# Performance work log

Hardware: AMD Instinct MI355X
Metric: run time of the kernel (lower is better)

Reference implementation:

```python
import jax, jax.numpy as jnp
import numpy as np

B, C, H, W = 8, 384, 32, 32
HEADS, DIM_HEAD = 6, 64
INNER = HEADS * DIM_HEAD  # 384


def setup_inputs() -> dict:
    key = jax.random.key(0)
    ks = jax.random.split(key, 6)
    s = 0.02
    return {
        "query": jax.random.normal(ks[0], (B, C, H, W), jnp.float32),
        "context": jax.random.normal(ks[1], (B, C, H, W), jnp.float32),
        "Wq": jax.random.normal(ks[2], (INNER, C), jnp.float32) * s,
        "Wk": jax.random.normal(ks[3], (INNER, C), jnp.float32) * s,
        "Wv": jax.random.normal(ks[4], (INNER, C), jnp.float32) * s,
        "Wo": jax.random.normal(ks[5], (C, INNER), jnp.float32) * s,
        "bo": jnp.zeros((C,), jnp.float32),
    }


def reference(query, context, Wq, Wk, Wv, Wo, bo):
    scale = DIM_HEAD ** (-0.5)
    b, _, h, w = query.shape
    n = h * w  # tokens
    # 1x1 convs == channel-wise linear projections
    q = jnp.einsum('bchw,oc->bohw', query, Wq)
    k = jnp.einsum('bchw,oc->bohw', context, Wk)
    v = jnp.einsum('bchw,oc->bohw', context, Wv)
    # split heads: [B, heads, dim_head, N]
    q = q.reshape(b, HEADS, DIM_HEAD, n)
    k = k.reshape(b, HEADS, DIM_HEAD, n)
    v = v.reshape(b, HEADS, DIM_HEAD, n)
    # attn[b,h,i,j] = sum_d q[b,h,d,i] k[b,h,d,j] * scale
    attn = jax.nn.softmax(jnp.einsum('bhdn,bhdm->bhnm', q, k) * scale, axis=-1)
    # out[b,h,i,d] = sum_j attn[b,h,i,j] v[b,h,d,j]
    out = jnp.einsum('bhnm,bhdm->bhdn', attn, v)  # [B, heads, dim_head, N]
    out = out.reshape(b, INNER, h, w)
    out = jnp.einsum('bchw,oc->bohw', out, Wo) + bo[None, :, None, None]
    attn_map = attn.mean(axis=(1, 2)).reshape(b, h, w)
    return out, attn_map
```

## Files before the change

kernel.cpp:

```cpp
#include <hip/hip_runtime.h>

#define BATCH 8
#define CCH   384
#define NTOK  1024
#define HEADS 6
#define DHEAD 64
#define QSCALE 0.18033688011112042f

typedef __bf16 bf16x8 __attribute__((ext_vector_type(8)));
typedef float  f32x4  __attribute__((ext_vector_type(4)));
typedef float  f32x2  __attribute__((ext_vector_type(2)));

#define MFMA16(a, b, c) __builtin_amdgcn_mfma_f32_16x16x32_bf16((a), (b), (c), 0, 0, 0)

__device__ __forceinline__ short f2b(float x) {
    unsigned u = __float_as_uint(x);
    u += 0x7fffu + ((u >> 16) & 1u);
    return (short)(u >> 16);
}

__device__ __forceinline__ void gld_lds16(const short* gp, short* lp) {
    __builtin_amdgcn_global_load_lds(
        (const __attribute__((address_space(1))) void*)gp,
        (__attribute__((address_space(3))) void*)lp, 16, 0, 0);
}

__device__ __forceinline__ void stage_tile(const short* gbase, size_t gstride,
                                           short* lbase, int wv, int lane) {
#pragma unroll
    for (int t = 0; t < 2; ++t) {
        const int row = t * 8 + (lane >> 3);
        const int c   = (lane & 7) ^ (row & 7);
        gld_lds16(gbase + (size_t)(wv * 16 + row) * gstride + c * 8,
                  lbase + (wv * 16 + t * 8) * 64);
    }
}
__device__ __forceinline__ bf16x8 frag_read(const short* lbase, int row, int c) {
    const int pc = c ^ (row & 7);
    return *(const bf16x8*)(lbase + row * 64 + pc * 8);
}

__device__ __forceinline__ void gemm128_core(
    const short* __restrict__ Ag, const short* __restrict__ Bg,
    short* Ast, short* Bst, f32x4 acc[4][4])
{
    const int tid = threadIdx.x, lane = tid & 63;
    const int l15 = tid & 15, quad = (tid >> 4) & 3, wv = tid >> 6;

    stage_tile(Ag, CCH, Ast, wv, lane);
    stage_tile(Ag + 64 * CCH, CCH, Ast + 4096, wv, lane);
    stage_tile(Bg, CCH, Bst, wv, lane);
    stage_tile(Bg + 64 * CCH, CCH, Bst + 4096, wv, lane);
    __syncthreads();

#pragma unroll
    for (int kc = 0; kc < 6; ++kc) {
        const int cur = kc & 1;
        if (kc < 5) {
            short* An = Ast + (cur ^ 1) * 8192;
            short* Bn = Bst + (cur ^ 1) * 8192;
            stage_tile(Ag + (kc + 1) * 64, CCH, An, wv, lane);
            stage_tile(Ag + (kc + 1) * 64 + 64 * CCH, CCH, An + 4096, wv, lane);
            stage_tile(Bg + (kc + 1) * 64, CCH, Bn, wv, lane);
            stage_tile(Bg + (kc + 1) * 64 + 64 * CCH, CCH, Bn + 4096, wv, lane);
        }
        const short* Atile = Ast + cur * 8192 + (wv >> 1) * 4096;
        const short* Btile = Bst + cur * 8192 + (wv & 1) * 4096;
#pragma unroll
        for (int h = 0; h < 2; ++h) {
            bf16x8 a[4], b[4];
#pragma unroll
            for (int s = 0; s < 4; ++s) {
                a[s] = frag_read(Atile, s * 16 + l15, h * 4 + quad);
                b[s] = frag_read(Btile, s * 16 + l15, h * 4 + quad);
            }
#pragma unroll
            for (int si = 0; si < 4; ++si)
#pragma unroll
                for (int sj = 0; sj < 4; ++sj)
                    acc[si][sj] = MFMA16(a[si], b[sj], acc[si][sj]);
        }
        __syncthreads();
    }
}

__device__ __forceinline__ void epilogue_bf16(
    f32x4 acc[4][4], short* cbuf,
    short* __restrict__ out, size_t obase, int ostride)
{
    const int tid = threadIdx.x;
    const int l15 = tid & 15, quad = (tid >> 4) & 3, wv = tid >> 6;
    const int wi = (wv >> 1) * 64, wj = (wv & 1) * 64;
    __syncthreads();
#pragma unroll
    for (int si = 0; si < 4; ++si)
#pragma unroll
        for (int sj = 0; sj < 4; ++sj)
#pragma unroll
            for (int rr = 0; rr < 4; ++rr)
                cbuf[(wi + si * 16 + quad * 4 + rr) * 128 + wj + sj * 16 + l15] =
                    f2b(acc[si][sj][rr]);
    __syncthreads();
#pragma unroll
    for (int pass = 0; pass < 8; ++pass) {
        const int row = pass * 16 + (tid >> 4);
        bf16x8 vchunk = *(const bf16x8*)(cbuf + row * 128 + l15 * 8);
        *(bf16x8*)(out + obase + (size_t)row * ostride + l15 * 8) = vchunk;
    }
}

__global__ __launch_bounds__(256) void prep(
    const float* __restrict__ Xq, const float* __restrict__ Xc,
    const float* __restrict__ w0, const float* __restrict__ w1,
    const float* __restrict__ w2, const float* __restrict__ w3,
    short* __restrict__ Xtq, short* __restrict__ Xtc,
    short* __restrict__ o0, short* __restrict__ o1,
    short* __restrict__ o2, short* __restrict__ o3,
    float* __restrict__ amap)
{
    __shared__ float tile[64][65];
    const int id = blockIdx.x, tid = threadIdx.x;
    if (id < 1536) {
        const int zz = id % 16, t = id / 16;
        const int n0 = (t % 16) * 64, c0 = (t / 16) * 64;
        const float* X = (zz < 8) ? Xq : Xc;
        short* Xt      = (zz < 8) ? Xtq : Xtc;
        const int b = zz & 7;
        const int tx = tid & 15, ty = tid >> 4;
#pragma unroll
        for (int rr = 0; rr < 4; ++rr) {
            const int c = rr * 16 + ty;
            float4 v = *(const float4*)&X[((size_t)(b * CCH + c0 + c)) * NTOK + n0 + tx * 4];
            tile[c][tx * 4 + 0] = v.x; tile[c][tx * 4 + 1] = v.y;
            tile[c][tx * 4 + 2] = v.z; tile[c][tx * 4 + 3] = v.w;
        }
        __syncthreads();
        const int n = tid >> 2, cb = (tid & 3) * 16;
        short tmp[16];
#pragma unroll
        for (int cc = 0; cc < 16; ++cc) tmp[cc] = f2b(tile[cb + cc][n]);
        short* dst = &Xt[((size_t)(b * NTOK + n0 + n)) * CCH + c0 + cb];
        *(int4*)dst = *(int4*)&tmp[0];
        *(int4*)(dst + 8) = *(int4*)&tmp[8];
    } else if (id < 2112) {
        const int w = id - 1536;
        const int which = w / 144;
        const int idx = (w % 144) * 256 + tid;
        const float* s = which == 0 ? w0 : which == 1 ? w1 : which == 2 ? w2 : w3;
        short* d       = which == 0 ? o0 : which == 1 ? o1 : which == 2 ? o2 : o3;
        float4 v = ((const float4*)s)[idx];
        short4 o = make_short4(f2b(v.x), f2b(v.y), f2b(v.z), f2b(v.w));
        ((short4*)d)[idx] = o;
    } else {
        const int o = (id - 2112) * 1024 + tid * 4;
        float4 z = {0.f, 0.f, 0.f, 0.f};
        *(float4*)&amap[o] = z;
    }
}

__global__ __launch_bounds__(256, 2) void gemm_qkv(
    const short* __restrict__ xtq, const short* __restrict__ xtc,
    const short* __restrict__ wq, const short* __restrict__ wk,
    const short* __restrict__ wvm,
    short* __restrict__ qout, short* __restrict__ kout, short* __restrict__ vout)
{
    __shared__ __align__(16) short Ast[2][8192];
    __shared__ __align__(16) short Bst[2][8192];
    const int id = blockIdx.x;
    const int b = id & 7, r = id >> 3;
    const int which = r / 24, tt = r % 24;

    const short *Ag, *Bg;
    short* out;
    size_t obase;
    int ostride;
    if (which < 2) {
        const int it = tt / 3, jt = tt % 3;
        const short* x = (which == 0) ? xtq : xtc;
        const short* W = (which == 0) ? wq : wk;
        Ag = x + ((size_t)(b * NTOK + it * 128)) * CCH;
        Bg = W + (size_t)(jt * 128) * CCH;
        out = (which == 0) ? qout : kout;
        obase = ((size_t)(b * NTOK + it * 128)) * CCH + jt * 128;
        ostride = CCH;
    } else {
        const int ct = tt % 3, nt = tt / 3;
        Ag = wvm + (size_t)(ct * 128) * CCH;
        Bg = xtc + ((size_t)(b * NTOK + nt * 128)) * CCH;
        out = vout;
        obase = ((size_t)(b * CCH + ct * 128)) * NTOK + nt * 128;
        ostride = NTOK;
    }

    f32x4 z4 = {0.f, 0.f, 0.f, 0.f};
    f32x4 acc[4][4];
#pragma unroll
    for (int si = 0; si < 4; ++si)
#pragma unroll
        for (int sj = 0; sj < 4; ++sj) acc[si][sj] = z4;

    gemm128_core(Ag, Bg, &Ast[0][0], &Bst[0][0], acc);

    if (which == 0) {
#pragma unroll
        for (int si = 0; si < 4; ++si)
#pragma unroll
            for (int sj = 0; sj < 4; ++sj)
#pragma unroll
                for (int rr = 0; rr < 4; ++rr)
                    acc[si][sj][rr] *= QSCALE;
    }
    epilogue_bf16(acc, &Ast[0][0], out, obase, ostride);
}

__global__ __launch_bounds__(256, 2) void o_proj(
    const short* __restrict__ wo, const short* __restrict__ omid,
    const float* __restrict__ bias, float* __restrict__ Y)
{
    __shared__ __align__(16) short Ast[2][8192];
    __shared__ __align__(16) short Bst[2][8192];
    const int id = blockIdx.x;
    const int b = id & 7, r = id >> 3;
    const int ct = r % 3, nt = r / 3;

    const short* Ag = wo + (size_t)(ct * 128) * CCH;
    const short* Bg = omid + ((size_t)(b * NTOK + nt * 128)) * CCH;

    f32x4 z4 = {0.f, 0.f, 0.f, 0.f};
    f32x4 acc[4][4];
#pragma unroll
    for (int si = 0; si < 4; ++si)
#pragma unroll
        for (int sj = 0; sj < 4; ++sj) acc[si][sj] = z4;

    gemm128_core(Ag, Bg, &Ast[0][0], &Bst[0][0], acc);

    const int tid = threadIdx.x;
    const int l15 = tid & 15, quad = (tid >> 4) & 3, wv = tid >> 6;
    const int wi = (wv >> 1) * 64, wj = (wv & 1) * 64;
#pragma unroll
    for (int si = 0; si < 4; ++si) {
#pragma unroll
        for (int rr = 0; rr < 4; ++rr) {
            const int ch = ct * 128 + wi + si * 16 + quad * 4 + rr;
            const float bv = bias[ch];
#pragma unroll
            for (int sj = 0; sj < 4; ++sj)
                Y[((size_t)(b * CCH + ch)) * NTOK + nt * 128 + wj + sj * 16 + l15] =
                    acc[si][sj][rr] + bv;
        }
    }
}

__global__ __launch_bounds__(256, 2) void attn(
    const short* __restrict__ qt, const short* __restrict__ kt,
    const short* __restrict__ vc, short* __restrict__ omid,
    float* __restrict__ amap)
{
    __shared__ __align__(16) short Kst[2][64 * 64];
    __shared__ __align__(16) short Vst[2][64 * 64];
    __shared__ __align__(16) short Pst[4][16][64];
    __shared__ float colbuf[4][1024];

    const int tid = threadIdx.x, lane = tid & 63;
    const int l15 = tid & 15, quad = (tid >> 4) & 3, wv = tid >> 6;
    const int id = blockIdx.x;
    const int b = id & 7, rr_ = id >> 3;
    const int h = rr_ % 6, i0 = (rr_ / 6) * 64;

    const size_t hoff = (size_t)b * NTOK * CCH + h * DHEAD;
    const short* Kg = kt + hoff;
    const short* Vg = vc + ((size_t)(b * CCH + h * DHEAD)) * NTOK;

    const short* qp = qt + hoff + (size_t)(i0 + wv * 16 + l15) * CCH + quad * 8;
    const bf16x8 qa0 = *(const bf16x8*)qp;
    const bf16x8 qa1 = *(const bf16x8*)(qp + 32);

    int ebuf[16][4];

    stage_tile(Kg, CCH, Kst[0], wv, lane);
    stage_tile(Vg, NTOK, Vst[0], wv, lane);
    __syncthreads();

    float den[4] = {0.f, 0.f, 0.f, 0.f};
    f32x4 z4o = {0.f, 0.f, 0.f, 0.f};
    f32x4 oacc[4] = {z4o, z4o, z4o, z4o};

#pragma unroll
    for (int jt = 0; jt < 16; ++jt) {
        const int cur = jt & 1;
        if (jt < 15) {
            stage_tile(Kg + (size_t)(jt + 1) * 64 * CCH, CCH, Kst[cur ^ 1], wv, lane);
            stage_tile(Vg + (size_t)(jt + 1) * 64, NTOK, Vst[cur ^ 1], wv, lane);
        }
        f32x4 s[4] = {z4o, z4o, z4o, z4o};
#pragma unroll
        for (int ns = 0; ns < 4; ++ns) {
            const int row = ns * 16 + l15;
            bf16x8 k0 = frag_read(Kst[cur], row, quad);
            bf16x8 k1 = frag_read(Kst[cur], row, quad + 4);
            s[ns] = MFMA16(qa0, k0, s[ns]);
            s[ns] = MFMA16(qa1, k1, s[ns]);
        }
#pragma unroll
        for (int ns = 0; ns < 4; ++ns) {
            const float e0 = exp2f(s[ns][0]);
            const float e1 = exp2f(s[ns][1]);
            const float e2 = exp2f(s[ns][2]);
            const float e3 = exp2f(s[ns][3]);
            den[0] += e0; den[1] += e1; den[2] += e2; den[3] += e3;
            int w = __builtin_amdgcn_cvt_pk_fp8_f32(e0, e1, 0, false);
            w = __builtin_amdgcn_cvt_pk_fp8_f32(e2, e3, w, true);
            ebuf[jt][ns] = w;
            const int c = ns * 2 + (l15 >> 3);
            const int r0 = quad * 4, r1 = r0 + 1, r2 = r0 + 2, r3 = r0 + 3;
            Pst[wv][r0][((c ^ (r0 & 7)) << 3) | (l15 & 7)] = f2b(e0);
            Pst[wv][r1][((c ^ (r1 & 7)) << 3) | (l15 & 7)] = f2b(e1);
            Pst[wv][r2][((c ^ (r2 & 7)) << 3) | (l15 & 7)] = f2b(e2);
            Pst[wv][r3][((c ^ (r3 & 7)) << 3) | (l15 & 7)] = f2b(e3);
        }
        asm volatile("" ::: "memory");
        const int pc0 = quad ^ (l15 & 7);
        const int pc1 = (quad + 4) ^ (l15 & 7);
        bf16x8 pa0 = *(const bf16x8*)&Pst[wv][l15][pc0 * 8];
        bf16x8 pa1 = *(const bf16x8*)&Pst[wv][l15][pc1 * 8];
        asm volatile("" ::: "memory");

#pragma unroll
        for (int ds = 0; ds < 4; ++ds) {
            const int row = ds * 16 + l15;
            bf16x8 v0 = frag_read(Vst[cur], row, quad);
            bf16x8 v1 = frag_read(Vst[cur], row, quad + 4);
            oacc[ds] = MFMA16(pa0, v0, oacc[ds]);
            oacc[ds] = MFMA16(pa1, v1, oacc[ds]);
        }
        __syncthreads();
    }

#pragma unroll
    for (int r = 0; r < 4; ++r) {
        den[r] += __shfl_xor(den[r], 1);
        den[r] += __shfl_xor(den[r], 2);
        den[r] += __shfl_xor(den[r], 4);
        den[r] += __shfl_xor(den[r], 8);
    }
    float rden[4];
#pragma unroll
    for (int r = 0; r < 4; ++r) rden[r] = 1.0f / den[r];

#pragma unroll
    for (int ds = 0; ds < 4; ++ds)
#pragma unroll
        for (int r = 0; r < 4; ++r) {
            const int i = i0 + wv * 16 + quad * 4 + r;
            omid[((size_t)(b * NTOK + i)) * CCH + h * DHEAD + ds * 16 + l15] =
                f2b(oacc[ds][r] * rden[r]);
        }

#pragma unroll
    for (int jt = 0; jt < 16; ++jt)
#pragma unroll
        for (int ns = 0; ns < 4; ++ns) {
            const f32x2 lo = __builtin_amdgcn_cvt_pk_f32_fp8(ebuf[jt][ns], false);
            const f32x2 hi = __builtin_amdgcn_cvt_pk_f32_fp8(ebuf[jt][ns], true);
            float cs = lo[0] * rden[0] + lo[1] * rden[1]
                     + hi[0] * rden[2] + hi[1] * rden[3];
            cs += __shfl_xor(cs, 16);
            cs += __shfl_xor(cs, 32);
            if (quad == 0) colbuf[wv][jt * 64 + ns * 16 + l15] = cs;
        }
    __syncthreads();
    for (int idx = tid; idx < 1024; idx += 256) {
        const float t = colbuf[0][idx] + colbuf[1][idx]
                      + colbuf[2][idx] + colbuf[3][idx];
        atomicAdd(amap + (size_t)b * NTOK + idx, t * (1.0f / (HEADS * NTOK)));
    }
}

extern "C" void kernel_launch(void* const* d_in, const int* in_sizes, int n_in,
                              void* d_out, int out_size, void* d_ws, size_t ws_size,
                              hipStream_t stream)
{
    const float* query   = (const float*)d_in[0];
    const float* context = (const float*)d_in[1];
    const float* Wq      = (const float*)d_in[2];
    const float* Wk      = (const float*)d_in[3];
    const float* Wv      = (const float*)d_in[4];
    const float* Wo      = (const float*)d_in[5];
    const float* bo      = (const float*)d_in[6];

    float* out = (float*)d_out;
    const size_t out_elems = (size_t)BATCH * CCH * NTOK;
    float* attn_map = out + out_elems;

    short* ws = (short*)d_ws;
    const size_t XT = (size_t)BATCH * NTOK * CCH;
    const size_t WSZ = (size_t)CCH * CCH;
    short* xtq  = ws;
    short* xtc  = xtq + XT;
    short* wqb  = xtc + XT;
    short* wkb  = wqb + WSZ;
    short* wvb  = wkb + WSZ;
    short* wob  = wvb + WSZ;
    short* qtb  = wob + WSZ;
    short* ktb  = qtb + XT;
    short* vcb  = ktb + XT;
    short* omid = vcb + XT;

    const dim3 blk(256);

    prep<<<dim3(2120), blk, 0, stream>>>(query, context, Wq, Wk, Wv, Wo,
                                         xtq, xtc, wqb, wkb, wvb, wob, attn_map);

    gemm_qkv<<<dim3(576), blk, 0, stream>>>(xtq, xtc, wqb, wkb, wvb,
                                            qtb, ktb, vcb);

    attn<<<dim3(768), blk, 0, stream>>>(qtb, ktb, vcb, omid, attn_map);

    o_proj<<<dim3(192), blk, 0, stream>>>(wob, omid, bo, out);
}
```

Measured before the change: 203.4 us.

## Split attention into two passes: denominator pass then normalized PV with streaming column sums

Replaces the single-pass kernel, which buffered unnormalized fp8 probabilities in registers (ebuf) for a later column-sum, with a two-pass scheme. The first pass recomputes QK^T to get the softmax denominators. The second pass recomputes QK^T, normalizes the probabilities, feeds them to the PV MFMA, and emits the attention-map column sums per tile with atomics. This removes the large register array and the 16 KB colbuf, and drops the two-blocks-per-SM launch bound, but it doubles the QK^T MFMA and exp work and the K loads.

```diff
diff --git a/kernel.cpp b/kernel.cpp
--- a/kernel.cpp
+++ b/kernel.cpp
@@ -9,7 +9,6 @@
 
 typedef __bf16 bf16x8 __attribute__((ext_vector_type(8)));
 typedef float  f32x4  __attribute__((ext_vector_type(4)));
-typedef float  f32x2  __attribute__((ext_vector_type(2)));
 
 #define MFMA16(a, b, c) __builtin_amdgcn_mfma_f32_16x16x32_bf16((a), (b), (c), 0, 0, 0)
 
@@ -252,7 +251,7 @@
     }
 }
 
-__global__ __launch_bounds__(256, 2) void attn(
+__global__ __launch_bounds__(256) void attn(
     const short* __restrict__ qt, const short* __restrict__ kt,
     const short* __restrict__ vc, short* __restrict__ omid,
     float* __restrict__ amap)
@@ -260,7 +259,7 @@
     __shared__ __align__(16) short Kst[2][64 * 64];
     __shared__ __align__(16) short Vst[2][64 * 64];
     __shared__ __align__(16) short Pst[4][16][64];
-    __shared__ float colbuf[4][1024];
+    __shared__ float colbuf[2][4][64];
 
     const int tid = threadIdx.x, lane = tid & 63;
     const int l15 = tid & 15, quad = (tid >> 4) & 3, wv = tid >> 6;
@@ -276,24 +275,16 @@
     const bf16x8 qa0 = *(const bf16x8*)qp;
     const bf16x8 qa1 = *(const bf16x8*)(qp + 32);
 
-    int ebuf[16][4];
-
     stage_tile(Kg, CCH, Kst[0], wv, lane);
-    stage_tile(Vg, NTOK, Vst[0], wv, lane);
     __syncthreads();
 
     float den[4] = {0.f, 0.f, 0.f, 0.f};
-    f32x4 z4o = {0.f, 0.f, 0.f, 0.f};
-    f32x4 oacc[4] = {z4o, z4o, z4o, z4o};
-
-#pragma unroll
     for (int jt = 0; jt < 16; ++jt) {
         const int cur = jt & 1;
-        if (jt < 15) {
+        if (jt < 15)
             stage_tile(Kg + (size_t)(jt + 1) * 64 * CCH, CCH, Kst[cur ^ 1], wv, lane);
-            stage_tile(Vg + (size_t)(jt + 1) * 64, NTOK, Vst[cur ^ 1], wv, lane);
-        }
-        f32x4 s[4] = {z4o, z4o, z4o, z4o};
+        f32x4 z4 = {0.f, 0.f, 0.f, 0.f};
+        f32x4 s[4] = {z4, z4, z4, z4};
 #pragma unroll
         for (int ns = 0; ns < 4; ++ns) {
             const int row = ns * 16 + l15;
@@ -303,21 +294,67 @@
             s[ns] = MFMA16(qa1, k1, s[ns]);
         }
 #pragma unroll
+        for (int ns = 0; ns < 4; ++ns)
+#pragma unroll
+            for (int r = 0; r < 4; ++r)
+                den[r] += exp2f(s[ns][r]);
+        __syncthreads();
+    }
+#pragma unroll
+    for (int r = 0; r < 4; ++r) {
+        den[r] += __shfl_xor(den[r], 1);
+        den[r] += __shfl_xor(den[r], 2);
+        den[r] += __shfl_xor(den[r], 4);
+        den[r] += __shfl_xor(den[r], 8);
+    }
+    float rden[4];
+#pragma unroll
+    for (int r = 0; r < 4; ++r) rden[r] = 1.0f / den[r];
+
+    stage_tile(Kg, CCH, Kst[0], wv, lane);
+    stage_tile(Vg, NTOK, Vst[0], wv, lane);
+    __syncthreads();
+
+    f32x4 z4o = {0.f, 0.f, 0.f, 0.f};
+    f32x4 oacc[4] = {z4o, z4o, z4o, z4o};
+    for (int jt = 0; jt < 16; ++jt) {
+        const int cur = jt & 1;
+        if (jt < 15) {
+            stage_tile(Kg + (size_t)(jt + 1) * 64 * CCH, CCH, Kst[cur ^ 1], wv, lane);
+            stage_tile(Vg + (size_t)(jt + 1) * 64, NTOK, Vst[cur ^ 1], wv, lane);
+        }
+        f32x4 s[4] = {z4o, z4o, z4o, z4o};
+#pragma unroll
         for (int ns = 0; ns < 4; ++ns) {
-            const float e0 = exp2f(s[ns][0]);
-            const float e1 = exp2f(s[ns][1]);
-            const float e2 = exp2f(s[ns][2]);
-            const float e3 = exp2f(s[ns][3]);
-            den[0] += e0; den[1] += e1; den[2] += e2; den[3] += e3;
-            int w = __builtin_amdgcn_cvt_pk_fp8_f32(e0, e1, 0, false);
-            w = __builtin_amdgcn_cvt_pk_fp8_f32(e2, e3, w, true);
-            ebuf[jt][ns] = w;
+            const int row = ns * 16 + l15;
+            bf16x8 k0 = frag_read(Kst[cur], row, quad);
+            bf16x8 k1 = frag_read(Kst[cur], row, quad + 4);
+            s[ns] = MFMA16(qa0, k0, s[ns]);
+            s[ns] = MFMA16(qa1, k1, s[ns]);
+        }
+        float p[4][4];
+#pragma unroll
+        for (int ns = 0; ns < 4; ++ns)
+#pragma unroll
+            for (int r = 0; r < 4; ++r)
+                p[ns][r] = exp2f(s[ns][r]) * rden[r];
+
+#pragma unroll
+        for (int ns = 0; ns < 4; ++ns) {
+            float cs = p[ns][0] + p[ns][1] + p[ns][2] + p[ns][3];
+            cs += __shfl_xor(cs, 16);
+            cs += __shfl_xor(cs, 32);
+            if (quad == 0) colbuf[cur][wv][ns * 16 + l15] = cs;
+        }
+
+#pragma unroll
+        for (int ns = 0; ns < 4; ++ns) {
             const int c = ns * 2 + (l15 >> 3);
-            const int r0 = quad * 4, r1 = r0 + 1, r2 = r0 + 2, r3 = r0 + 3;
-            Pst[wv][r0][((c ^ (r0 & 7)) << 3) | (l15 & 7)] = f2b(e0);
-            Pst[wv][r1][((c ^ (r1 & 7)) << 3) | (l15 & 7)] = f2b(e1);
-            Pst[wv][r2][((c ^ (r2 & 7)) << 3) | (l15 & 7)] = f2b(e2);
-            Pst[wv][r3][((c ^ (r3 & 7)) << 3) | (l15 & 7)] = f2b(e3);
+#pragma unroll
+            for (int r = 0; r < 4; ++r) {
+                const int row = quad * 4 + r;
+                Pst[wv][row][((c ^ (row & 7)) << 3) | (l15 & 7)] = f2b(p[ns][r]);
+            }
         }
         asm volatile("" ::: "memory");
         const int pc0 = quad ^ (l15 & 7);
@@ -335,18 +372,13 @@
             oacc[ds] = MFMA16(pa1, v1, oacc[ds]);
         }
         __syncthreads();
-    }
-
-#pragma unroll
-    for (int r = 0; r < 4; ++r) {
-        den[r] += __shfl_xor(den[r], 1);
-        den[r] += __shfl_xor(den[r], 2);
-        den[r] += __shfl_xor(den[r], 4);
-        den[r] += __shfl_xor(den[r], 8);
-    }
-    float rden[4];
-#pragma unroll
-    for (int r = 0; r < 4; ++r) rden[r] = 1.0f / den[r];
+        if (tid < 64) {
+            const float t = colbuf[cur][0][tid] + colbuf[cur][1][tid]
+                          + colbuf[cur][2][tid] + colbuf[cur][3][tid];
+            atomicAdd(amap + (size_t)b * NTOK + jt * 64 + tid,
+                      t * (1.0f / (HEADS * NTOK)));
+        }
+    }
 
 #pragma unroll
     for (int ds = 0; ds < 4; ++ds)
@@ -354,27 +386,8 @@
         for (int r = 0; r < 4; ++r) {
             const int i = i0 + wv * 16 + quad * 4 + r;
             omid[((size_t)(b * NTOK + i)) * CCH + h * DHEAD + ds * 16 + l15] =
-                f2b(oacc[ds][r] * rden[r]);
-        }
-
-#pragma unroll
-    for (int jt = 0; jt < 16; ++jt)
-#pragma unroll
-        for (int ns = 0; ns < 4; ++ns) {
-            const f32x2 lo = __builtin_amdgcn_cvt_pk_f32_fp8(ebuf[jt][ns], false);
-            const f32x2 hi = __builtin_amdgcn_cvt_pk_f32_fp8(ebuf[jt][ns], true);
-            float cs = lo[0] * rden[0] + lo[1] * rden[1]
-                     + hi[0] * rden[2] + hi[1] * rden[3];
-            cs += __shfl_xor(cs, 16);
-            cs += __shfl_xor(cs, 32);
-            if (quad == 0) colbuf[wv][jt * 64 + ns * 16 + l15] = cs;
-        }
-    __syncthreads();
-    for (int idx = tid; idx < 1024; idx += 256) {
-        const float t = colbuf[0][idx] + colbuf[1][idx]
-                      + colbuf[2][idx] + colbuf[3][idx];
-        atomicAdd(amap + (size_t)b * NTOK + idx, t * (1.0f / (HEADS * NTOK)));
-    }
+                f2b(oacc[ds][r]);
+        }
 }
 
 extern "C" void kernel_launch(void* const* d_in, const int* in_sizes, int n_in,
```

Measured after the change: 167.3 us. 1.22x faster.
